# Optimization experiments

Measured on AMD Instinct MI355X. Metric: run time of the kernel, lower is better.

## Reference

```python
import jax, jax.numpy as jnp
import numpy as np

NUM_EXPERTS = 8
HIDDEN = 2048
INTER = 4096
TOKENS = 8192
TOP_K = 2


def setup_inputs() -> dict:
    key = jax.random.key(0)
    ks = jax.random.split(key, 5)
    s = 0.02
    return {
        "x": jax.random.normal(ks[0], (TOKENS, HIDDEN), dtype=jnp.float32),
        "gate_w": jax.random.normal(ks[1], (NUM_EXPERTS, HIDDEN), dtype=jnp.float32) * s,
        "w1": jax.random.normal(ks[2], (NUM_EXPERTS, INTER, HIDDEN), dtype=jnp.float32) * s,
        "w2": jax.random.normal(ks[3], (NUM_EXPERTS, HIDDEN, INTER), dtype=jnp.float32) * s,
        "w3": jax.random.normal(ks[4], (NUM_EXPERTS, INTER, HIDDEN), dtype=jnp.float32) * s,
    }


def reference(x, gate_w, w1, w2, w3):
    # Router: softmax over experts in fp32, then top-2 (no renormalization,
    # matching the torch module which uses the raw top-k softmax probs).
    router_logits = jnp.einsum("th,eh->te", x, gate_w)  # [T, E]
    probs = jax.nn.softmax(router_logits.astype(jnp.float32), axis=1)
    topk_w, topk_idx = jax.lax.top_k(probs, TOP_K)  # [T, K]
    topk_w = topk_w.astype(x.dtype)

    num_experts = w1.shape[0]
    out = jnp.zeros_like(x)
    for e in range(num_experts):
        # Combined routing coefficient for expert e per token (0 if unrouted).
        coef = jnp.sum(jnp.where(topk_idx == e, topk_w, 0.0), axis=1)  # [T]
        # SwiGLU expert FFN: down(silu(gate(x)) * up(x))
        g = jnp.einsum("th,ih->ti", x, w1[e])
        u = jnp.einsum("th,ih->ti", x, w3[e])
        h = jax.nn.silu(g) * u
        y = jnp.einsum("ti,hi->th", h, w2[e])
        out = out + coef[:, None] * y
    return out
```

## Files before the change

### kernel.cpp

```cpp
#include <hip/hip_runtime.h>
#include <stdint.h>
#include <stddef.h>


constexpr int kTokens  = 8192;
constexpr int kHidden  = 2048;
constexpr int kInter   = 4096;
constexpr int kExperts = 8;

constexpr int BM = 128, BN = 128, BK = 64;
constexpr int MAX_MT = (2 * kTokens) / BM + kExperts;

constexpr int BM2 = 256, BN2 = 128, BK2 = 64;
constexpr int MAX_MT2 = (2 * kTokens) / BM2 + kExperts;
constexpr int NT2 = kHidden / BK2;

typedef short bf16x8 __attribute__((ext_vector_type(8)));
typedef float f32x4  __attribute__((ext_vector_type(4)));
typedef unsigned int u32;

__device__ __forceinline__ unsigned short f2bf(float f) {
  union { float f; unsigned u; } v; v.f = f;
  unsigned r = v.u + 0x7FFFu + ((v.u >> 16) & 1u);
  return (unsigned short)(r >> 16);
}

__device__ __forceinline__ void gload16(const void* g, void* l) {
  __builtin_amdgcn_global_load_lds(
      (const __attribute__((address_space(1))) u32*)g,
      (__attribute__((address_space(3))) u32*)l, 16, 0, 0);
}

__global__ __launch_bounds__(256) void convert_w(
    const float* __restrict__ src, unsigned short* __restrict__ dst,
    int lp, int lq, int K, long nchunks)
{
  long stride = (long)gridDim.x * blockDim.x;
  for (long g = blockIdx.x * (long)blockDim.x + threadIdx.x; g < nchunks; g += stride) {
    int  l   = (int)(g & 1023);
    long blk = g >> 10;
    int  q   = (int)(blk & ((1 << lq) - 1));
    long ep  = blk >> lq;
    int  p   = (int)(ep & ((1 << lp) - 1));
    int  e   = (int)(ep >> lp);
    int r = l >> 3, cs = l & 7, c = cs ^ (r & 7);
    size_t soff = (((size_t)(e << lp) + p) * 128 + r) * (size_t)K + (size_t)q * 64 + c * 8;
    float4 v0 = *reinterpret_cast<const float4*>(src + soff);
    float4 v1 = *reinterpret_cast<const float4*>(src + soff + 4);
    uint4 o;
    o.x = (u32)f2bf(v0.x) | ((u32)f2bf(v0.y) << 16);
    o.y = (u32)f2bf(v0.z) | ((u32)f2bf(v0.w) << 16);
    o.z = (u32)f2bf(v1.x) | ((u32)f2bf(v1.y) << 16);
    o.w = (u32)f2bf(v1.z) | ((u32)f2bf(v1.w) << 16);
    *reinterpret_cast<uint4*>(dst + g * 8) = o;
  }
}

__global__ __launch_bounds__(256) void moe_router(
    const float* __restrict__ x, const float* __restrict__ gate_w,
    unsigned short* __restrict__ xb, int* __restrict__ counts,
    int* __restrict__ list_idx, float* __restrict__ list_w)
{
  const int lane = threadIdx.x & 63;
  const int wave = threadIdx.x >> 6;
  const int t = blockIdx.x * 4 + wave;

  float acc[kExperts];
#pragma unroll
  for (int e = 0; e < kExperts; ++e) acc[e] = 0.f;

  const float4* xrow = reinterpret_cast<const float4*>(x + (size_t)t * kHidden);
#pragma unroll
  for (int j = 0; j < 8; ++j) {
    float4 xv = xrow[j * 64 + lane];
    uint2 pk;
    pk.x = (u32)f2bf(xv.x) | ((u32)f2bf(xv.y) << 16);
    pk.y = (u32)f2bf(xv.z) | ((u32)f2bf(xv.w) << 16);
    *reinterpret_cast<uint2*>(xb + (size_t)t * kHidden + j * 256 + lane * 4) = pk;
#pragma unroll
    for (int e = 0; e < kExperts; ++e) {
      float4 gv = reinterpret_cast<const float4*>(gate_w + (size_t)e * kHidden)[j * 64 + lane];
      acc[e] += xv.x * gv.x + xv.y * gv.y + xv.z * gv.z + xv.w * gv.w;
    }
  }
#pragma unroll
  for (int e = 0; e < kExperts; ++e) {
#pragma unroll
    for (int m = 32; m >= 1; m >>= 1) acc[e] += __shfl_xor(acc[e], m);
  }
  if (lane == 0) {
    float mx = acc[0];
#pragma unroll
    for (int e = 1; e < kExperts; ++e) mx = fmaxf(mx, acc[e]);
    float p[kExperts]; float s = 0.f;
#pragma unroll
    for (int e = 0; e < kExperts; ++e) { p[e] = __expf(acc[e] - mx); s += p[e]; }
    float inv = 1.f / s;
    int i1 = 0; float v1 = p[0];
#pragma unroll
    for (int e = 1; e < kExperts; ++e) if (p[e] > v1) { v1 = p[e]; i1 = e; }
    int i2 = (i1 == 0) ? 1 : 0; float v2 = p[i2];
#pragma unroll
    for (int e = 0; e < kExperts; ++e) {
      if (e == i1 || e == i2) continue;
      if (p[e] > v2) { v2 = p[e]; i2 = e; }
    }
    int s1 = atomicAdd(&counts[i1], 1);
    list_idx[i1 * kTokens + s1] = t;
    list_w [i1 * kTokens + s1] = v1 * inv;
    int s2 = atomicAdd(&counts[i2], 1);
    list_idx[i2 * kTokens + s2] = t;
    list_w [i2 * kTokens + s2] = v2 * inv;
  }
}

__device__ __forceinline__ bool map_tile(const int* __restrict__ counts, int mt,
                                         int& e, int& lm, int& sb, int& ne)
{
  int tb = 0; sb = 0;
  for (e = 0; e < kExperts; ++e) {
    ne = counts[e];
    int tiles = (ne + BM - 1) / BM;
    if (mt < tb + tiles) { lm = mt - tb; return true; }
    tb += tiles; sb += ne;
  }
  return false;
}

__device__ __forceinline__ bool map_tile2(const int* __restrict__ counts, int mt,
                                          int& e, int& lm, int& sb, int& ne)
{
  int tb = 0; sb = 0;
  for (e = 0; e < kExperts; ++e) {
    ne = counts[e];
    int tiles = (ne + BM2 - 1) / BM2;
    if (mt < tb + tiles) { lm = mt - tb; return true; }
    tb += tiles; sb += ne;
  }
  return false;
}

__global__ __launch_bounds__(512, 2) void moe_gu2(
    const unsigned short* __restrict__ xb,
    const unsigned short* __restrict__ w1b, const unsigned short* __restrict__ w3b,
    const int* __restrict__ counts, const int* __restrict__ list_idx,
    unsigned short* __restrict__ hbuf)
{
  __shared__ unsigned short lds[65536];
  __shared__ int toks[BM2];

  const int tid = threadIdx.x;
  const int nt  = blockIdx.x / MAX_MT2;
  const int mt  = blockIdx.x % MAX_MT2;

  int e, lm, sb, ne;
  if (!map_tile2(counts, mt, e, lm, sb, ne)) return;
  const int row0 = lm * BM2;

  if (tid < BM2) {
    int lr = row0 + tid;
    toks[tid] = list_idx[e * kTokens + ((lr < ne) ? lr : 0)];
  }
  __syncthreads();

  const int lane = tid & 63;
  const int w    = tid >> 6;
  const int wr   = w >> 2;
  const int wc   = w & 3;

  const unsigned short* srcA[2][2];
  const unsigned short* srcB1[2];
  const unsigned short* srcB3[2];
  {
    const size_t bb = ((size_t)(e * (kInter / BN2) + nt) * (kHidden / BK2)) * 1024;
#pragma unroll
    for (int i = 0; i < 2; ++i) {
      int l = (w * 2 + i) * 64 + lane;
      int r = l >> 3, cs = l & 7, c = cs ^ (r & 7);
#pragma unroll
      for (int h = 0; h < 2; ++h)
        srcA[h][i] = xb + (size_t)toks[h * 128 + r] * kHidden + c * 8;
      srcB1[i] = w1b + (bb + l) * 8;
      srcB3[i] = w3b + (bb + l) * 8;
    }
  }

  f32x4 accG[8][2], accU[8][2];
  const f32x4 zero = {0.f, 0.f, 0.f, 0.f};
#pragma unroll
  for (int m = 0; m < 8; ++m)
#pragma unroll
    for (int n = 0; n < 2; ++n) { accG[m][n] = zero; accU[m][n] = zero; }

#pragma unroll
  for (int i = 0; i < 2; ++i) gload16(srcA[0][i], &lds[0 * 8192 + (w * 2 + i) * 512]);
#pragma unroll
  for (int i = 0; i < 2; ++i) gload16(srcA[1][i], &lds[1 * 8192 + (w * 2 + i) * 512]);
#pragma unroll
  for (int i = 0; i < 2; ++i) gload16(srcB1[i], &lds[32768 + (w * 2 + i) * 512]);
#pragma unroll
  for (int i = 0; i < 2; ++i) gload16(srcB3[i], &lds[49152 + (w * 2 + i) * 512]);
  asm volatile("s_waitcnt vmcnt(2)" ::: "memory");
  __builtin_amdgcn_sched_barrier(0);
  __builtin_amdgcn_s_barrier();

  for (int t = 0; t < NT2; ++t) {
    const int cb = t & 1, nb = cb ^ 1;
    const int tn = (t + 1 < NT2) ? (t + 1) : (NT2 - 1);
    const int Acur = (cb * 2 + wr) * 8192;
    const int B1c  = 32768 + cb * 8192;
    const int B3c  = 49152 + cb * 8192;
    const int An0  = (nb * 2 + 0) * 8192;
    const int An1  = (nb * 2 + 1) * 8192;
    const int B1n  = 32768 + nb * 8192;
    const int B3n  = 49152 + nb * 8192;

    bf16x8 a0[4][2], a1[4][2];
    {
      bf16x8 b1f[2][2];
#pragma unroll
      for (int m = 0; m < 4; ++m) {
        const int r = m * 16 + (lane & 15);
#pragma unroll
        for (int kk = 0; kk < 2; ++kk) {
          const int cq = kk * 4 + (lane >> 4);
          a0[m][kk] = *reinterpret_cast<const bf16x8*>(&lds[Acur + r * 64 + ((cq ^ (r & 7)) << 3)]);
        }
      }
#pragma unroll
      for (int n = 0; n < 2; ++n) {
        const int r = wc * 32 + n * 16 + (lane & 15);
#pragma unroll
        for (int kk = 0; kk < 2; ++kk) {
          const int cq = kk * 4 + (lane >> 4);
          b1f[n][kk] = *reinterpret_cast<const bf16x8*>(&lds[B1c + r * 64 + ((cq ^ (r & 7)) << 3)]);
        }
      }
#pragma unroll
      for (int i = 0; i < 2; ++i) gload16(srcA[0][i] + tn * 64, &lds[An0 + (w * 2 + i) * 512]);
      __builtin_amdgcn_s_setprio(1);
#pragma unroll
      for (int m = 0; m < 4; ++m)
#pragma unroll
        for (int n = 0; n < 2; ++n)
#pragma unroll
          for (int kk = 0; kk < 2; ++kk)
            accG[m][n] = __builtin_amdgcn_mfma_f32_16x16x32_bf16(a0[m][kk], b1f[n][kk], accG[m][n], 0, 0, 0);
      __builtin_amdgcn_s_setprio(0);
      __builtin_amdgcn_sched_barrier(0);
      __builtin_amdgcn_s_barrier();

#pragma unroll
      for (int m = 0; m < 4; ++m) {
        const int r = 64 + m * 16 + (lane & 15);
#pragma unroll
        for (int kk = 0; kk < 2; ++kk) {
          const int cq = kk * 4 + (lane >> 4);
          a1[m][kk] = *reinterpret_cast<const bf16x8*>(&lds[Acur + r * 64 + ((cq ^ (r & 7)) << 3)]);
        }
      }
#pragma unroll
      for (int i = 0; i < 2; ++i) gload16(srcA[1][i] + tn * 64, &lds[An1 + (w * 2 + i) * 512]);
      __builtin_amdgcn_s_setprio(1);
#pragma unroll
      for (int m = 0; m < 4; ++m)
#pragma unroll
        for (int n = 0; n < 2; ++n)
#pragma unroll
          for (int kk = 0; kk < 2; ++kk)
            accG[4 + m][n] = __builtin_amdgcn_mfma_f32_16x16x32_bf16(a1[m][kk], b1f[n][kk], accG[4 + m][n], 0, 0, 0);
      __builtin_amdgcn_s_setprio(0);
      __builtin_amdgcn_sched_barrier(0);
      asm volatile("s_waitcnt vmcnt(4)" ::: "memory");
      __builtin_amdgcn_s_barrier();
    }
    {
      bf16x8 b3f[2][2];
#pragma unroll
      for (int n = 0; n < 2; ++n) {
        const int r = wc * 32 + n * 16 + (lane & 15);
#pragma unroll
        for (int kk = 0; kk < 2; ++kk) {
          const int cq = kk * 4 + (lane >> 4);
          b3f[n][kk] = *reinterpret_cast<const bf16x8*>(&lds[B3c + r * 64 + ((cq ^ (r & 7)) << 3)]);
        }
      }
#pragma unroll
      for (int i = 0; i < 2; ++i) gload16(srcB1[i] + (size_t)tn * 8192, &lds[B1n + (w * 2 + i) * 512]);
      __builtin_amdgcn_s_setprio(1);
#pragma unroll
      for (int m = 0; m < 4; ++m)
#pragma unroll
        for (int n = 0; n < 2; ++n)
#pragma unroll
          for (int kk = 0; kk < 2; ++kk)
            accU[m][n] = __builtin_amdgcn_mfma_f32_16x16x32_bf16(a0[m][kk], b3f[n][kk], accU[m][n], 0, 0, 0);
      __builtin_amdgcn_s_setprio(0);
      __builtin_amdgcn_sched_barrier(0);
      __builtin_amdgcn_s_barrier();

#pragma unroll
      for (int i = 0; i < 2; ++i) gload16(srcB3[i] + (size_t)tn * 8192, &lds[B3n + (w * 2 + i) * 512]);
      __builtin_amdgcn_s_setprio(1);
#pragma unroll
      for (int m = 0; m < 4; ++m)
#pragma unroll
        for (int n = 0; n < 2; ++n)
#pragma unroll
          for (int kk = 0; kk < 2; ++kk)
            accU[4 + m][n] = __builtin_amdgcn_mfma_f32_16x16x32_bf16(a1[m][kk], b3f[n][kk], accU[4 + m][n], 0, 0, 0);
      __builtin_amdgcn_s_setprio(0);
      __builtin_amdgcn_sched_barrier(0);
      asm volatile("s_waitcnt vmcnt(2)" ::: "memory");
      __builtin_amdgcn_s_barrier();
    }
  }

#pragma unroll
  for (int am = 0; am < 8; ++am) {
#pragma unroll
    for (int r = 0; r < 4; ++r) {
      int rloc = wr * 128 + am * 16 + ((lane >> 4) * 4) + r;
      int lrow = row0 + rloc;
      if (lrow < ne) {
        size_t base = (size_t)(sb + lrow) * kInter + (size_t)nt * BN2 + wc * 32 + (lane & 15);
#pragma unroll
        for (int n = 0; n < 2; ++n) {
          float g = accG[am][n][r];
          float u = accU[am][n][r];
          float hv = (g / (1.f + __expf(-g))) * u;
          hbuf[base + n * 16] = f2bf(hv);
        }
      }
    }
  }
}

__global__ __launch_bounds__(256, 3) void moe_y(
    const unsigned short* __restrict__ hbuf,
    const unsigned short* __restrict__ w2b,
    const int* __restrict__ counts, const int* __restrict__ list_idx,
    const float* __restrict__ list_w,
    float* __restrict__ out)
{
  __shared__ unsigned short As[BM * BK];
  __shared__ unsigned short Bs[BN * BK];
  __shared__ int   toks[BM];
  __shared__ float cofs[BM];

  const int tid = threadIdx.x;
  const int nt  = blockIdx.x / MAX_MT;
  const int mt  = blockIdx.x % MAX_MT;

  int e, lm, sb, ne;
  if (!map_tile(counts, mt, e, lm, sb, ne)) return;
  const int row0 = lm * BM;

  if (tid < BM) {
    int lr = row0 + tid;
    bool v = lr < ne;
    toks[tid] = v ? list_idx[e * kTokens + lr] : 0;
    cofs[tid] = v ? list_w [e * kTokens + lr] : 0.f;
  }
  __syncthreads();

  const int lane = tid & 63;
  const int w = tid >> 6;
  const int wr = w >> 1, wc = w & 1;

  const unsigned short* srcA[4];
  const unsigned short* srcB2[4];
  const size_t bbase = ((size_t)(e * (kHidden / BN) + nt) * (kInter / BK)) * 1024;
#pragma unroll
  for (int i = 0; i < 4; ++i) {
    int l = (w * 4 + i) * 64 + lane;
    int r = l >> 3, cs = l & 7, c = cs ^ (r & 7);
    srcA[i]  = hbuf + (size_t)(sb + row0 + r) * kInter + c * 8;
    srcB2[i] = w2b  + (bbase + l) * 8;
  }

  f32x4 acc[4][4];
  const f32x4 zero = {0.f, 0.f, 0.f, 0.f};
#pragma unroll
  for (int m = 0; m < 4; ++m)
#pragma unroll
    for (int n = 0; n < 4; ++n) acc[m][n] = zero;

  for (int ks = 0; ks < kInter / BK; ++ks) {
#pragma unroll
    for (int i = 0; i < 4; ++i) {
      gload16(srcA[i]  + ks * BK,           &As[(w * 4 + i) * 512]);
      gload16(srcB2[i] + (size_t)ks * 8192, &Bs[(w * 4 + i) * 512]);
    }
    __syncthreads();
#pragma unroll
    for (int kk = 0; kk < 2; ++kk) {
      const int cq = kk * 4 + (lane >> 4);
      bf16x8 a[4], b[4];
#pragma unroll
      for (int m = 0; m < 4; ++m) {
        int row = wr * 64 + m * 16 + (lane & 15);
        a[m] = *reinterpret_cast<const bf16x8*>(&As[row * 64 + ((cq ^ (row & 7)) << 3)]);
      }
#pragma unroll
      for (int n = 0; n < 4; ++n) {
        int row = wc * 64 + n * 16 + (lane & 15);
        b[n] = *reinterpret_cast<const bf16x8*>(&Bs[row * 64 + ((cq ^ (row & 7)) << 3)]);
      }
#pragma unroll
      for (int m = 0; m < 4; ++m)
#pragma unroll
        for (int n = 0; n < 4; ++n)
          acc[m][n] = __builtin_amdgcn_mfma_f32_16x16x32_bf16(a[m], b[n], acc[m][n], 0, 0, 0);
    }
    __syncthreads();
  }

#pragma unroll
  for (int m = 0; m < 4; ++m) {
#pragma unroll
    for (int r = 0; r < 4; ++r) {
      int rloc = wr * 64 + m * 16 + ((lane >> 4) * 4) + r;
      if (row0 + rloc < ne) {
        float cf = cofs[rloc];
        size_t obase = (size_t)toks[rloc] * kHidden + (size_t)nt * BN + wc * 64 + (lane & 15);
#pragma unroll
        for (int n = 0; n < 4; ++n)
          atomicAdd(&out[obase + n * 16], cf * acc[m][n][r]);
      }
    }
  }
}

__global__ __launch_bounds__(256, 2) void moe_gu_f32(
    const unsigned short* __restrict__ xb,
    const float* __restrict__ w1, const float* __restrict__ w3,
    const int* __restrict__ counts, const int* __restrict__ list_idx,
    unsigned short* __restrict__ hbuf)
{
  __shared__ unsigned short As [BM * BK];
  __shared__ unsigned short B1s[BN * BK];
  __shared__ unsigned short B3s[BN * BK];
  __shared__ int toks[BM];

  const int tid = threadIdx.x;
  const int nt  = blockIdx.x / MAX_MT;
  const int mt  = blockIdx.x % MAX_MT;

  int e, lm, sb, ne;
  if (!map_tile(counts, mt, e, lm, sb, ne)) return;
  const int row0 = lm * BM;

  if (tid < BM) {
    int lr = row0 + tid;
    toks[tid] = list_idx[e * kTokens + ((lr < ne) ? lr : 0)];
  }
  __syncthreads();

  const unsigned short* aptr[4];
#pragma unroll
  for (int i = 0; i < 4; ++i) {
    int chunk = i * 256 + tid;
    int r = chunk >> 3, c8 = chunk & 7;
    aptr[i] = xb + (size_t)toks[r] * kHidden + c8 * 8;
  }
  const float* w1e = w1 + (size_t)e * kInter * kHidden;
  const float* w3e = w3 + (size_t)e * kInter * kHidden;

  f32x4 accG[4][4], accU[4][4];
  const f32x4 zero = {0.f, 0.f, 0.f, 0.f};
#pragma unroll
  for (int m = 0; m < 4; ++m)
#pragma unroll
    for (int n = 0; n < 4; ++n) { accG[m][n] = zero; accU[m][n] = zero; }

  const int lane = tid & 63;
  const int wr = (tid >> 6) >> 1;
  const int wc = (tid >> 6) & 1;

  for (int k0 = 0; k0 < kHidden; k0 += BK) {
#pragma unroll
    for (int i = 0; i < 4; ++i) {
      int chunk = i * 256 + tid;
      uint4 v = *reinterpret_cast<const uint4*>(aptr[i] + k0);
      *reinterpret_cast<uint4*>(&As[chunk * 8]) = v;
    }
#pragma unroll
    for (int i = 0; i < 8; ++i) {
      int c = i * 256 + tid;
      int rowB = c >> 4, c16 = c & 15;
      size_t off = ((size_t)(nt * BN + rowB)) * kHidden + k0 + c16 * 4;
      float4 v1 = *reinterpret_cast<const float4*>(w1e + off);
      float4 v3 = *reinterpret_cast<const float4*>(w3e + off);
      uint2 p1, p3;
      p1.x = (u32)f2bf(v1.x) | ((u32)f2bf(v1.y) << 16);
      p1.y = (u32)f2bf(v1.z) | ((u32)f2bf(v1.w) << 16);
      p3.x = (u32)f2bf(v3.x) | ((u32)f2bf(v3.y) << 16);
      p3.y = (u32)f2bf(v3.z) | ((u32)f2bf(v3.w) << 16);
      *reinterpret_cast<uint2*>(&B1s[rowB * BK + c16 * 4]) = p1;
      *reinterpret_cast<uint2*>(&B3s[rowB * BK + c16 * 4]) = p3;
    }
    __syncthreads();
#pragma unroll
    for (int kk = 0; kk < 2; ++kk) {
      const int klo = kk * 32 + (lane >> 4) * 8;
      bf16x8 a[4], b1v[4], b3v[4];
#pragma unroll
      for (int m = 0; m < 4; ++m)
        a[m] = *reinterpret_cast<const bf16x8*>(&As[(wr * 64 + m * 16 + (lane & 15)) * BK + klo]);
#pragma unroll
      for (int n = 0; n < 4; ++n) {
// ... 72 lines not shown
  const int wc = (tid >> 6) & 1;

  for (int k0 = 0; k0 < kInter; k0 += BK) {
#pragma unroll
    for (int i = 0; i < 4; ++i) {
      int chunk = i * 256 + tid;
      int r = chunk >> 3, c8 = chunk & 7;
      uint4 v = *reinterpret_cast<const uint4*>(arow + (size_t)r * kInter + k0 + c8 * 8);
      *reinterpret_cast<uint4*>(&As[chunk * 8]) = v;
    }
#pragma unroll
    for (int i = 0; i < 8; ++i) {
      int c = i * 256 + tid;
      int rowB = c >> 4, c16 = c & 15;
      size_t off = ((size_t)(nt * BN + rowB)) * kInter + k0 + c16 * 4;
      float4 v2 = *reinterpret_cast<const float4*>(w2e + off);
      uint2 p2;
      p2.x = (u32)f2bf(v2.x) | ((u32)f2bf(v2.y) << 16);
      p2.y = (u32)f2bf(v2.z) | ((u32)f2bf(v2.w) << 16);
      *reinterpret_cast<uint2*>(&Bs[rowB * BK + c16 * 4]) = p2;
    }
    __syncthreads();
#pragma unroll
    for (int kk = 0; kk < 2; ++kk) {
      const int klo = kk * 32 + (lane >> 4) * 8;
      bf16x8 a[4], b[4];
#pragma unroll
      for (int m = 0; m < 4; ++m)
        a[m] = *reinterpret_cast<const bf16x8*>(&As[(wr * 64 + m * 16 + (lane & 15)) * BK + klo]);
#pragma unroll
      for (int n = 0; n < 4; ++n)
        b[n] = *reinterpret_cast<const bf16x8*>(&Bs[(wc * 64 + n * 16 + (lane & 15)) * BK + klo]);
#pragma unroll
      for (int m = 0; m < 4; ++m)
#pragma unroll
        for (int n = 0; n < 4; ++n)
          acc[m][n] = __builtin_amdgcn_mfma_f32_16x16x32_bf16(a[m], b[n], acc[m][n], 0, 0, 0);
    }
    __syncthreads();
  }
#pragma unroll
  for (int m = 0; m < 4; ++m) {
#pragma unroll
    for (int r = 0; r < 4; ++r) {
      int rloc = wr * 64 + m * 16 + ((lane >> 4) * 4) + r;
      if (row0 + rloc < ne) {
        float cf = cofs[rloc];
        size_t obase = (size_t)toks[rloc] * kHidden + (size_t)nt * BN + wc * 64 + (lane & 15);
#pragma unroll
        for (int n = 0; n < 4; ++n)
          atomicAdd(&out[obase + n * 16], cf * acc[m][n][r]);
      }
    }
  }
}

extern "C" void kernel_launch(void* const* d_in, const int* in_sizes, int n_in,
                              void* d_out, int out_size, void* d_ws, size_t ws_size,
                              hipStream_t stream)
{
  const float* x      = (const float*)d_in[0];
  const float* gate_w = (const float*)d_in[1];
  const float* w1     = (const float*)d_in[2];
  const float* w2     = (const float*)d_in[3];
  const float* w3     = (const float*)d_in[4];
  float* out = (float*)d_out;

  char* ws = (char*)d_ws;
  const size_t MiB = 1ull << 20;
  int*   counts   = (int*)(ws);
  int*   list_idx = (int*)(ws + 1024);
  float* list_w   = (float*)(ws + 1024 + kExperts * kTokens * 4);

  hipMemsetAsync(counts, 0, 1024, stream);
  hipMemsetAsync(out, 0, (size_t)kTokens * kHidden * sizeof(float), stream);

  if (ws_size >= 418 * MiB) {
    unsigned short* xb   = (unsigned short*)(ws + 1 * MiB);
    unsigned short* w1b  = (unsigned short*)(ws + 33 * MiB);
    unsigned short* w3b  = (unsigned short*)(ws + 161 * MiB);
    unsigned short* hbuf = (unsigned short*)(ws + 289 * MiB);
    unsigned short* w2b  = w1b;

    const long nch = (long)kExperts * (kInter / BN) * (kHidden / BK) * 1024;
    convert_w<<<4096, 256, 0, stream>>>(w1, w1b, 5, 5, kHidden, nch);
    convert_w<<<4096, 256, 0, stream>>>(w3, w3b, 5, 5, kHidden, nch);
    moe_router<<<kTokens / 4, 256, 0, stream>>>(x, gate_w, xb, counts, list_idx, list_w);
    moe_gu2<<<(kInter / BN2) * MAX_MT2, 512, 0, stream>>>(xb, w1b, w3b, counts, list_idx, hbuf);
    convert_w<<<4096, 256, 0, stream>>>(w2, w2b, 4, 6, kInter, nch);
    moe_y<<<(kHidden / BN) * MAX_MT, 256, 0, stream>>>(hbuf, w2b, counts, list_idx, list_w, out);
  } else {
    unsigned short* xb   = (unsigned short*)(ws + 1 * MiB);
    unsigned short* hbuf = (unsigned short*)(ws + 36 * MiB);
    moe_router<<<kTokens / 4, 256, 0, stream>>>(x, gate_w, xb, counts, list_idx, list_w);
    moe_gu_f32<<<(kInter / BN) * MAX_MT, 256, 0, stream>>>(xb, w1, w3, counts, list_idx, hbuf);
    moe_y_f32 <<<(kHidden / BN) * MAX_MT, 256, 0, stream>>>(hbuf, w2, counts, list_idx, list_w, out);
  }
}
```

Measured before the change: 1.492 ms.

## Pipeline down-projection with 256-row tiles, triple-buffered LDS, and reordered grid

Replaces the down-projection kernel with a 512-thread, 256x128 tile version. It uses triple-buffered LDS, async global-to-LDS prefetch two steps ahead, and one barrier per k-step instead of two syncthreads. The gate/up kernel is unrolled by two with fewer barriers and a reordered prefetch schedule. Both grids now put the N panel as the fast index, so blocks sharing the same token rows run together and reuse them from cache. This gives more overlap and reuse, but raises register and LDS pressure, and the fixed vmcnt counts must match the reordered loads.

Result: slower. 1.797 ms (median of 2 runs) (+20.5%).

```diff
diff --git a/kernel.cpp b/kernel.cpp
--- a/kernel.cpp
+++ b/kernel.cpp
@@ -11,9 +11,13 @@
 constexpr int BM = 128, BN = 128, BK = 64;
 constexpr int MAX_MT = (2 * kTokens) / BM + kExperts;
 
-constexpr int BM2 = 256, BN2 = 128, BK2 = 64;
+constexpr int BM2 = 256, BN2 = 128;
 constexpr int MAX_MT2 = (2 * kTokens) / BM2 + kExperts;
-constexpr int NT2 = kHidden / BK2;
+constexpr int NT2 = kHidden / BK;
+constexpr int NTY = kInter / BK;
+constexpr int NPAN_GU = kInter / BN2;
+constexpr int NPAN_Y  = kHidden / BN2;
+constexpr int kSlotCap = 16512;
 
 typedef short bf16x8 __attribute__((ext_vector_type(8)));
 typedef float f32x4  __attribute__((ext_vector_type(4)));
@@ -150,8 +154,8 @@
   __shared__ int toks[BM2];
 
   const int tid = threadIdx.x;
-  const int nt  = blockIdx.x / MAX_MT2;
-  const int mt  = blockIdx.x % MAX_MT2;
+  const int nt  = blockIdx.x % NPAN_GU;
+  const int mt  = blockIdx.x / NPAN_GU;
 
   int e, lm, sb, ne;
   if (!map_tile2(counts, mt, e, lm, sb, ne)) return;
@@ -172,7 +176,7 @@
   const unsigned short* srcB1[2];
   const unsigned short* srcB3[2];
   {
-    const size_t bb = ((size_t)(e * (kInter / BN2) + nt) * (kHidden / BK2)) * 1024;
+    const size_t bb = ((size_t)(e * NPAN_GU + nt) * NT2) * 1024;
 #pragma unroll
     for (int i = 0; i < 2; ++i) {
       int l = (w * 2 + i) * 64 + lane;
@@ -204,20 +208,22 @@
   __builtin_amdgcn_sched_barrier(0);
   __builtin_amdgcn_s_barrier();
 
-  for (int t = 0; t < NT2; ++t) {
-    const int cb = t & 1, nb = cb ^ 1;
-    const int tn = (t + 1 < NT2) ? (t + 1) : (NT2 - 1);
-    const int Acur = (cb * 2 + wr) * 8192;
-    const int B1c  = 32768 + cb * 8192;
-    const int B3c  = 49152 + cb * 8192;
-    const int An0  = (nb * 2 + 0) * 8192;
-    const int An1  = (nb * 2 + 1) * 8192;
-    const int B1n  = 32768 + nb * 8192;
-    const int B3n  = 49152 + nb * 8192;
-
-    bf16x8 a0[4][2], a1[4][2];
-    {
-      bf16x8 b1f[2][2];
+  for (int t2 = 0; t2 < NT2; t2 += 2) {
+#pragma unroll
+    for (int u = 0; u < 2; ++u) {
+      const int t  = t2 + u;
+      const int cb = u, nb = u ^ 1;
+      const int tn = (t + 1 < NT2) ? (t + 1) : (NT2 - 1);
+      const int Acur = (cb * 2 + wr) * 8192;
+      const int B1c  = 32768 + cb * 8192;
+      const int B3c  = 49152 + cb * 8192;
+      const int An0  = (nb * 2 + 0) * 8192;
+      const int An1  = (nb * 2 + 1) * 8192;
+      const int B1n  = 32768 + nb * 8192;
+      const int B3n  = 49152 + nb * 8192;
+
+      bf16x8 a0[4][2], a1[4][2], b1f[2][2], b3f[2][2];
+
 #pragma unroll
       for (int m = 0; m < 4; ++m) {
         const int r = m * 16 + (lane & 15);
@@ -237,7 +243,10 @@
         }
       }
 #pragma unroll
-      for (int i = 0; i < 2; ++i) gload16(srcA[0][i] + tn * 64, &lds[An0 + (w * 2 + i) * 512]);
+      for (int i = 0; i < 2; ++i) {
+        gload16(srcA[0][i] + tn * BK, &lds[An0 + (w * 2 + i) * 512]);
+        gload16(srcA[1][i] + tn * BK, &lds[An1 + (w * 2 + i) * 512]);
+      }
       __builtin_amdgcn_s_setprio(1);
 #pragma unroll
       for (int m = 0; m < 4; ++m)
@@ -248,7 +257,6 @@
             accG[m][n] = __builtin_amdgcn_mfma_f32_16x16x32_bf16(a0[m][kk], b1f[n][kk], accG[m][n], 0, 0, 0);
       __builtin_amdgcn_s_setprio(0);
       __builtin_amdgcn_sched_barrier(0);
-      __builtin_amdgcn_s_barrier();
 
 #pragma unroll
       for (int m = 0; m < 4; ++m) {
@@ -260,7 +268,8 @@
         }
       }
 #pragma unroll
-      for (int i = 0; i < 2; ++i) gload16(srcA[1][i] + tn * 64, &lds[An1 + (w * 2 + i) * 512]);
+      for (int i = 0; i < 2; ++i)
+        gload16(srcB1[i] + (size_t)tn * 8192, &lds[B1n + (w * 2 + i) * 512]);
       __builtin_amdgcn_s_setprio(1);
 #pragma unroll
       for (int m = 0; m < 4; ++m)
@@ -271,11 +280,9 @@
             accG[4 + m][n] = __builtin_amdgcn_mfma_f32_16x16x32_bf16(a1[m][kk], b1f[n][kk], accG[4 + m][n], 0, 0, 0);
       __builtin_amdgcn_s_setprio(0);
       __builtin_amdgcn_sched_barrier(0);
-      asm volatile("s_waitcnt vmcnt(4)" ::: "memory");
+      asm volatile("s_waitcnt vmcnt(6)" ::: "memory");
       __builtin_amdgcn_s_barrier();
-    }
-    {
-      bf16x8 b3f[2][2];
+
 #pragma unroll
       for (int n = 0; n < 2; ++n) {
         const int r = wc * 32 + n * 16 + (lane & 15);
@@ -286,7 +293,8 @@
         }
       }
 #pragma unroll
-      for (int i = 0; i < 2; ++i) gload16(srcB1[i] + (size_t)tn * 8192, &lds[B1n + (w * 2 + i) * 512]);
+      for (int i = 0; i < 2; ++i)
+        gload16(srcB3[i] + (size_t)tn * 8192, &lds[B3n + (w * 2 + i) * 512]);
       __builtin_amdgcn_s_setprio(1);
 #pragma unroll
       for (int m = 0; m < 4; ++m)
@@ -297,10 +305,6 @@
             accU[m][n] = __builtin_amdgcn_mfma_f32_16x16x32_bf16(a0[m][kk], b3f[n][kk], accU[m][n], 0, 0, 0);
       __builtin_amdgcn_s_setprio(0);
       __builtin_amdgcn_sched_barrier(0);
-      __builtin_amdgcn_s_barrier();
-
-#pragma unroll
-      for (int i = 0; i < 2; ++i) gload16(srcB3[i] + (size_t)tn * 8192, &lds[B3n + (w * 2 + i) * 512]);
       __builtin_amdgcn_s_setprio(1);
 #pragma unroll
       for (int m = 0; m < 4; ++m)
@@ -336,27 +340,94 @@
   }
 }
 
-__global__ __launch_bounds__(256, 3) void moe_y(
+#define Y_TILE(T, CB)                                                          \
+  {                                                                            \
+    const int tn  = ((T) + 2 < NTY) ? ((T) + 2) : (NTY - 1);                   \
+    const int cob = (CB) * 24576;                                              \
+    const int nxb = (((CB) + 2) % 3) * 24576;                                  \
+    bf16x8 a0[4][2], a1[4][2], bfv[2][2];                                      \
+    _Pragma("unroll")                                                          \
+    for (int m = 0; m < 4; ++m) {                                              \
+      const int r = m * 16 + (lane & 15);                                      \
+      _Pragma("unroll")                                                        \
+      for (int kk = 0; kk < 2; ++kk) {                                         \
+        const int cq = kk * 4 + (lane >> 4);                                   \
+        a0[m][kk] = *reinterpret_cast<const bf16x8*>(                          \
+            &lds[cob + wr * 8192 + r * 64 + ((cq ^ (r & 7)) << 3)]);           \
+      }                                                                        \
+    }                                                                          \
+    _Pragma("unroll")                                                          \
+    for (int n = 0; n < 2; ++n) {                                              \
+      const int r = wc * 32 + n * 16 + (lane & 15);                            \
+      _Pragma("unroll")                                                        \
+      for (int kk = 0; kk < 2; ++kk) {                                         \
+        const int cq = kk * 4 + (lane >> 4);                                   \
+        bfv[n][kk] = *reinterpret_cast<const bf16x8*>(                         \
+            &lds[cob + 16384 + r * 64 + ((cq ^ (r & 7)) << 3)]);               \
+      }                                                                        \
+    }                                                                          \
+    _Pragma("unroll")                                                          \
+    for (int i = 0; i < 2; ++i) {                                              \
+      gload16(srcA[0][i] + (size_t)tn * BK, &lds[nxb + (w * 2 + i) * 512]);    \
+      gload16(srcB[i] + (size_t)tn * 8192, &lds[nxb + 16384 + (w * 2 + i) * 512]); \
+    }                                                                          \
+    __builtin_amdgcn_s_setprio(1);                                             \
+    _Pragma("unroll")                                                          \
+    for (int m = 0; m < 4; ++m)                                                \
+      _Pragma("unroll")                                                        \
+      for (int n = 0; n < 2; ++n)                                              \
+        _Pragma("unroll")                                                      \
+        for (int kk = 0; kk < 2; ++kk)                                         \
+          acc[m][n] = __builtin_amdgcn_mfma_f32_16x16x32_bf16(a0[m][kk], bfv[n][kk], acc[m][n], 0, 0, 0); \
+    __builtin_amdgcn_s_setprio(0);                                             \
+    __builtin_amdgcn_sched_barrier(0);                                         \
+    _Pragma("unroll")                                                          \
+    for (int m = 0; m < 4; ++m) {                                              \
+      const int r = 64 + m * 16 + (lane & 15);                                 \
+      _Pragma("unroll")                                                        \
+      for (int kk = 0; kk < 2; ++kk) {                                         \
+        const int cq = kk * 4 + (lane >> 4);                                   \
+        a1[m][kk] = *reinterpret_cast<const bf16x8*>(                          \
+            &lds[cob + wr * 8192 + r * 64 + ((cq ^ (r & 7)) << 3)]);           \
+      }                                                                        \
+    }                                                                          \
+    _Pragma("unroll")                                                          \
+    for (int i = 0; i < 2; ++i)                                                \
+      gload16(srcA[1][i] + (size_t)tn * BK, &lds[nxb + 8192 + (w * 2 + i) * 512]); \
+    __builtin_amdgcn_s_setprio(1);                                             \
+    _Pragma("unroll")                                                          \
+    for (int m = 0; m < 4; ++m)                                                \
+      _Pragma("unroll")                                                        \
+      for (int n = 0; n < 2; ++n)                                              \
+        _Pragma("unroll")                                                      \
+        for (int kk = 0; kk < 2; ++kk)                                         \
+          acc[4 + m][n] = __builtin_amdgcn_mfma_f32_16x16x32_bf16(a1[m][kk], bfv[n][kk], acc[4 + m][n], 0, 0, 0); \
+    __builtin_amdgcn_s_setprio(0);                                             \
+    __builtin_amdgcn_sched_barrier(0);                                         \
+    asm volatile("s_waitcnt vmcnt(6)" ::: "memory");                           \
+    __builtin_amdgcn_s_barrier();                                              \
+  }
+
+__global__ __launch_bounds__(512, 2) void moe_y2(
     const unsigned short* __restrict__ hbuf,
     const unsigned short* __restrict__ w2b,
     const int* __restrict__ counts, const int* __restrict__ list_idx,
     const float* __restrict__ list_w,
     float* __restrict__ out)
 {
-  __shared__ unsigned short As[BM * BK];
-  __shared__ unsigned short Bs[BN * BK];
-  __shared__ int   toks[BM];
-  __shared__ float cofs[BM];
+  __shared__ unsigned short lds[73728];
+  __shared__ int   toks[BM2];
+  __shared__ float cofs[BM2];
 
   const int tid = threadIdx.x;
-  const int nt  = blockIdx.x / MAX_MT;
-  const int mt  = blockIdx.x % MAX_MT;
+  const int nt  = blockIdx.x % NPAN_Y;
+  const int mt  = blockIdx.x / NPAN_Y;
 
   int e, lm, sb, ne;
-  if (!map_tile(counts, mt, e, lm, sb, ne)) return;
-  const int row0 = lm * BM;
-
-  if (tid < BM) {
+  if (!map_tile2(counts, mt, e, lm, sb, ne)) return;
+  const int row0 = lm * BM2;
+
+  if (tid < BM2) {
     int lr = row0 + tid;
     bool v = lr < ne;
     toks[tid] = v ? list_idx[e * kTokens + lr] : 0;
@@ -365,68 +436,69 @@
   __syncthreads();
 
   const int lane = tid & 63;
-  const int w = tid >> 6;
-  const int wr = w >> 1, wc = w & 1;
-
-  const unsigned short* srcA[4];
-  const unsigned short* srcB2[4];
-  const size_t bbase = ((size_t)(e * (kHidden / BN) + nt) * (kInter / BK)) * 1024;
-#pragma unroll
-  for (int i = 0; i < 4; ++i) {
-    int l = (w * 4 + i) * 64 + lane;
-    int r = l >> 3, cs = l & 7, c = cs ^ (r & 7);
-    srcA[i]  = hbuf + (size_t)(sb + row0 + r) * kInter + c * 8;
-    srcB2[i] = w2b  + (bbase + l) * 8;
-  }
-
-  f32x4 acc[4][4];
+  const int w    = tid >> 6;
+  const int wr   = w >> 2;
+  const int wc   = w & 3;
+
+  const unsigned short* srcA[2][2];
+  const unsigned short* srcB[2];
+  {
+    const size_t bb = ((size_t)(e * NPAN_Y + nt) * NTY) * 1024;
+#pragma unroll
+    for (int i = 0; i < 2; ++i) {
+      int l = (w * 2 + i) * 64 + lane;
+      int r = l >> 3, cs = l & 7, c = cs ^ (r & 7);
+#pragma unroll
+      for (int h = 0; h < 2; ++h) {
+        int rg = sb + row0 + h * 128 + r;
+        if (rg > kSlotCap - 1) rg = kSlotCap - 1;
+        srcA[h][i] = hbuf + (size_t)rg * kInter + c * 8;
+      }
+      srcB[i] = w2b + (bb + l) * 8;
+    }
+  }
+
+  f32x4 acc[8][2];
   const f32x4 zero = {0.f, 0.f, 0.f, 0.f};
 #pragma unroll
-  for (int m = 0; m < 4; ++m)
-#pragma unroll
-    for (int n = 0; n < 4; ++n) acc[m][n] = zero;
-
-  for (int ks = 0; ks < kInter / BK; ++ks) {
-#pragma unroll
-    for (int i = 0; i < 4; ++i) {
-      gload16(srcA[i]  + ks * BK,           &As[(w * 4 + i) * 512]);
-      gload16(srcB2[i] + (size_t)ks * 8192, &Bs[(w * 4 + i) * 512]);
-    }
-    __syncthreads();
-#pragma unroll
-    for (int kk = 0; kk < 2; ++kk) {
-      const int cq = kk * 4 + (lane >> 4);
-      bf16x8 a[4], b[4];
-#pragma unroll
-      for (int m = 0; m < 4; ++m) {
-        int row = wr * 64 + m * 16 + (lane & 15);
-        a[m] = *reinterpret_cast<const bf16x8*>(&As[row * 64 + ((cq ^ (row & 7)) << 3)]);
-      }
-#pragma unroll
-      for (int n = 0; n < 4; ++n) {
-        int row = wc * 64 + n * 16 + (lane & 15);
-        b[n] = *reinterpret_cast<const bf16x8*>(&Bs[row * 64 + ((cq ^ (row & 7)) << 3)]);
-      }
-#pragma unroll
-      for (int m = 0; m < 4; ++m)
-#pragma unroll
-        for (int n = 0; n < 4; ++n)
-          acc[m][n] = __builtin_amdgcn_mfma_f32_16x16x32_bf16(a[m], b[n], acc[m][n], 0, 0, 0);
-    }
-    __syncthreads();
-  }
-
-#pragma unroll
-  for (int m = 0; m < 4; ++m) {
+  for (int m = 0; m < 8; ++m)
+#pragma unroll
+    for (int n = 0; n < 2; ++n) acc[m][n] = zero;
+
+#pragma unroll
+  for (int t = 0; t < 2; ++t) {
+    const int bo = t * 24576;
+#pragma unroll
+    for (int i = 0; i < 2; ++i) {
+      gload16(srcA[0][i] + (size_t)t * BK, &lds[bo + (w * 2 + i) * 512]);
+      gload16(srcB[i] + (size_t)t * 8192, &lds[bo + 16384 + (w * 2 + i) * 512]);
+    }
+#pragma unroll
+    for (int i = 0; i < 2; ++i)
+      gload16(srcA[1][i] + (size_t)t * BK, &lds[bo + 8192 + (w * 2 + i) * 512]);
+  }
+  asm volatile("s_waitcnt vmcnt(6)" ::: "memory");
+  __builtin_amdgcn_sched_barrier(0);
+  __builtin_amdgcn_s_barrier();
+
+  Y_TILE(0, 0)
+  for (int t3 = 1; t3 < NTY; t3 += 3) {
+    Y_TILE(t3, 1)
+    Y_TILE(t3 + 1, 2)
+    Y_TILE(t3 + 2, 0)
+  }
+
+#pragma unroll
+  for (int am = 0; am < 8; ++am) {
 #pragma unroll
     for (int r = 0; r < 4; ++r) {
-      int rloc = wr * 64 + m * 16 + ((lane >> 4) * 4) + r;
+      int rloc = wr * 128 + am * 16 + ((lane >> 4) * 4) + r;
       if (row0 + rloc < ne) {
         float cf = cofs[rloc];
-        size_t obase = (size_t)toks[rloc] * kHidden + (size_t)nt * BN + wc * 64 + (lane & 15);
-#pragma unroll
-        for (int n = 0; n < 4; ++n)
-          atomicAdd(&out[obase + n * 16], cf * acc[m][n][r]);
+        size_t obase = (size_t)toks[rloc] * kHidden + (size_t)nt * BN2 + wc * 32 + (lane & 15);
+#pragma unroll
+        for (int n = 0; n < 2; ++n)
+          atomicAdd(&out[obase + n * 16], cf * acc[am][n][r]);
       }
     }
   }
@@ -669,9 +741,9 @@
     convert_w<<<4096, 256, 0, stream>>>(w1, w1b, 5, 5, kHidden, nch);
     convert_w<<<4096, 256, 0, stream>>>(w3, w3b, 5, 5, kHidden, nch);
     moe_router<<<kTokens / 4, 256, 0, stream>>>(x, gate_w, xb, counts, list_idx, list_w);
-    moe_gu2<<<(kInter / BN2) * MAX_MT2, 512, 0, stream>>>(xb, w1b, w3b, counts, list_idx, hbuf);
+    moe_gu2<<<MAX_MT2 * NPAN_GU, 512, 0, stream>>>(xb, w1b, w3b, counts, list_idx, hbuf);
     convert_w<<<4096, 256, 0, stream>>>(w2, w2b, 4, 6, kInter, nch);
-    moe_y<<<(kHidden / BN) * MAX_MT, 256, 0, stream>>>(hbuf, w2b, counts, list_idx, list_w, out);
+    moe_y2<<<MAX_MT2 * NPAN_Y, 512, 0, stream>>>(hbuf, w2b, counts, list_idx, list_w, out);
   } else {
     unsigned short* xb   = (unsigned short*)(ws + 1 * MiB);
     unsigned short* hbuf = (unsigned short*)(ws + 36 * MiB);
```

## Pre-layout weights in MFMA fragment order and stream B operands straight to registers

Applied to the files above, without the earlier changes.

Weight conversion now writes bf16 weights in MFMA fragment order, so each lane can load its B fragments directly from global memory into registers. This removes the LDS staging for weights in both GEMMs. The gate/up kernel issues gate and up MFMAs interleaved in a single double-buffered loop, with only the activations double-buffered in LDS. The down-projection kernel moves to 256-row tiles with 512 threads and uses the same register-prefetch scheme. The cost is higher register pressure and uncoalesced-per-wave-but-contiguous global weight reads that rely on cache reuse across blocks.

Measured after the change: 1.587 ms. +6.4%, slower.

```diff
diff --git a/kernel.cpp b/kernel.cpp
--- a/kernel.cpp
+++ b/kernel.cpp
@@ -11,9 +11,13 @@
 constexpr int BM = 128, BN = 128, BK = 64;
 constexpr int MAX_MT = (2 * kTokens) / BM + kExperts;
 
-constexpr int BM2 = 256, BN2 = 128, BK2 = 64;
+constexpr int BM2 = 256, BN2 = 128;
 constexpr int MAX_MT2 = (2 * kTokens) / BM2 + kExperts;
-constexpr int NT2 = kHidden / BK2;
+constexpr int NT2 = kHidden / BK;
+constexpr int NTY = kInter / BK;
+constexpr int NPAN_GU = kInter / BN2;
+constexpr int NPAN_Y  = kHidden / BN2;
+constexpr int kSlotCap = 16512;
 
 typedef short bf16x8 __attribute__((ext_vector_type(8)));
 typedef float f32x4  __attribute__((ext_vector_type(4)));
@@ -31,20 +35,23 @@
       (__attribute__((address_space(3))) u32*)l, 16, 0, 0);
 }
 
-__global__ __launch_bounds__(256) void convert_w(
+__global__ __launch_bounds__(256) void convert_w_frag(
     const float* __restrict__ src, unsigned short* __restrict__ dst,
     int lp, int lq, int K, long nchunks)
 {
   long stride = (long)gridDim.x * blockDim.x;
   for (long g = blockIdx.x * (long)blockDim.x + threadIdx.x; g < nchunks; g += stride) {
-    int  l   = (int)(g & 1023);
+    int  c13 = (int)(g & 1023);
     long blk = g >> 10;
     int  q   = (int)(blk & ((1 << lq) - 1));
     long ep  = blk >> lq;
     int  p   = (int)(ep & ((1 << lp) - 1));
     int  e   = (int)(ep >> lp);
-    int r = l >> 3, cs = l & 7, c = cs ^ (r & 7);
-    size_t soff = (((size_t)(e << lp) + p) * 128 + r) * (size_t)K + (size_t)q * 64 + c * 8;
+    int fg = c13 >> 6, l = c13 & 63;
+    int g8 = fg >> 1, kk = fg & 1;
+    int row = g8 * 16 + (l & 15);
+    int kq  = kk * 4 + (l >> 4);
+    size_t soff = (((size_t)(e << lp) + p) * 128 + row) * (size_t)K + (size_t)q * 64 + kq * 8;
     float4 v0 = *reinterpret_cast<const float4*>(src + soff);
     float4 v1 = *reinterpret_cast<const float4*>(src + soff + 4);
     uint4 o;
@@ -140,13 +147,13 @@
   return false;
 }
 
-__global__ __launch_bounds__(512, 2) void moe_gu2(
+__global__ __launch_bounds__(512, 2) void moe_gu3(
     const unsigned short* __restrict__ xb,
     const unsigned short* __restrict__ w1b, const unsigned short* __restrict__ w3b,
     const int* __restrict__ counts, const int* __restrict__ list_idx,
     unsigned short* __restrict__ hbuf)
 {
-  __shared__ unsigned short lds[65536];
+  __shared__ unsigned short As[2][16384];
   __shared__ int toks[BM2];
 
   const int tid = threadIdx.x;
@@ -168,22 +175,21 @@
   const int wr   = w >> 2;
   const int wc   = w & 3;
 
-  const unsigned short* srcA[2][2];
-  const unsigned short* srcB1[2];
-  const unsigned short* srcB3[2];
-  {
-    const size_t bb = ((size_t)(e * (kInter / BN2) + nt) * (kHidden / BK2)) * 1024;
-#pragma unroll
-    for (int i = 0; i < 2; ++i) {
-      int l = (w * 2 + i) * 64 + lane;
-      int r = l >> 3, cs = l & 7, c = cs ^ (r & 7);
-#pragma unroll
-      for (int h = 0; h < 2; ++h)
-        srcA[h][i] = xb + (size_t)toks[h * 128 + r] * kHidden + c * 8;
-      srcB1[i] = w1b + (bb + l) * 8;
-      srcB3[i] = w3b + (bb + l) * 8;
-    }
-  }
+  const unsigned short* srcA[4];
+#pragma unroll
+  for (int i = 0; i < 4; ++i) {
+    int l = (w * 4 + i) * 64 + lane;
+    int r = l >> 3, c = (l & 7) ^ (r & 7);
+    srcA[i] = xb + (size_t)toks[r] * kHidden + c * 8;
+  }
+
+  const size_t tb0 = ((size_t)(e * NPAN_GU + nt)) * NT2 * 8192;
+  int foff[2][2];
+#pragma unroll
+  for (int n = 0; n < 2; ++n)
+#pragma unroll
+    for (int kk = 0; kk < 2; ++kk)
+      foff[n][kk] = (((wc * 2 + n) * 2 + kk) * 64 + lane) * 8;
 
   f32x4 accG[8][2], accU[8][2];
   const f32x4 zero = {0.f, 0.f, 0.f, 0.f};
@@ -192,128 +198,71 @@
 #pragma unroll
     for (int n = 0; n < 2; ++n) { accG[m][n] = zero; accU[m][n] = zero; }
 
-#pragma unroll
-  for (int i = 0; i < 2; ++i) gload16(srcA[0][i], &lds[0 * 8192 + (w * 2 + i) * 512]);
-#pragma unroll
-  for (int i = 0; i < 2; ++i) gload16(srcA[1][i], &lds[1 * 8192 + (w * 2 + i) * 512]);
-#pragma unroll
-  for (int i = 0; i < 2; ++i) gload16(srcB1[i], &lds[32768 + (w * 2 + i) * 512]);
-#pragma unroll
-  for (int i = 0; i < 2; ++i) gload16(srcB3[i], &lds[49152 + (w * 2 + i) * 512]);
-  asm volatile("s_waitcnt vmcnt(2)" ::: "memory");
+  bf16x8 b1a[2][2], b3a[2][2], b1b[2][2], b3b[2][2];
+
+#pragma unroll
+  for (int i = 0; i < 4; ++i) gload16(srcA[i], &As[0][(w * 4 + i) * 512]);
+  __builtin_amdgcn_sched_barrier(0);
+#pragma unroll
+  for (int n = 0; n < 2; ++n)
+#pragma unroll
+    for (int kk = 0; kk < 2; ++kk) {
+      b1a[n][kk] = *reinterpret_cast<const bf16x8*>(w1b + tb0 + foff[n][kk]);
+      b3a[n][kk] = *reinterpret_cast<const bf16x8*>(w3b + tb0 + foff[n][kk]);
+    }
+  asm volatile("s_waitcnt vmcnt(8)" ::: "memory");
   __builtin_amdgcn_sched_barrier(0);
   __builtin_amdgcn_s_barrier();
 
-  for (int t = 0; t < NT2; ++t) {
-    const int cb = t & 1, nb = cb ^ 1;
+  auto tile = [&](int t, int buf,
+                  bf16x8 (&b1c)[2][2], bf16x8 (&b3c)[2][2],
+                  bf16x8 (&b1n)[2][2], bf16x8 (&b3n)[2][2]) {
     const int tn = (t + 1 < NT2) ? (t + 1) : (NT2 - 1);
-    const int Acur = (cb * 2 + wr) * 8192;
-    const int B1c  = 32768 + cb * 8192;
-    const int B3c  = 49152 + cb * 8192;
-    const int An0  = (nb * 2 + 0) * 8192;
-    const int An1  = (nb * 2 + 1) * 8192;
-    const int B1n  = 32768 + nb * 8192;
-    const int B3n  = 49152 + nb * 8192;
-
-    bf16x8 a0[4][2], a1[4][2];
-    {
-      bf16x8 b1f[2][2];
+#pragma unroll
+    for (int i = 0; i < 4; ++i)
+      gload16(srcA[i] + tn * BK, &As[buf ^ 1][(w * 4 + i) * 512]);
+    __builtin_amdgcn_sched_barrier(0);
+    const size_t tbn = tb0 + (size_t)tn * 8192;
+#pragma unroll
+    for (int n = 0; n < 2; ++n)
+#pragma unroll
+      for (int kk = 0; kk < 2; ++kk) {
+        b1n[n][kk] = *reinterpret_cast<const bf16x8*>(w1b + tbn + foff[n][kk]);
+        b3n[n][kk] = *reinterpret_cast<const bf16x8*>(w3b + tbn + foff[n][kk]);
+      }
+#pragma unroll
+    for (int mh = 0; mh < 2; ++mh) {
+      bf16x8 a[4][2];
 #pragma unroll
       for (int m = 0; m < 4; ++m) {
-        const int r = m * 16 + (lane & 15);
+        const int r = wr * 128 + mh * 64 + m * 16 + (lane & 15);
 #pragma unroll
         for (int kk = 0; kk < 2; ++kk) {
           const int cq = kk * 4 + (lane >> 4);
-          a0[m][kk] = *reinterpret_cast<const bf16x8*>(&lds[Acur + r * 64 + ((cq ^ (r & 7)) << 3)]);
+          a[m][kk] = *reinterpret_cast<const bf16x8*>(
+              &As[buf][r * 64 + ((cq ^ (r & 7)) << 3)]);
         }
       }
 #pragma unroll
-      for (int n = 0; n < 2; ++n) {
-        const int r = wc * 32 + n * 16 + (lane & 15);
-#pragma unroll
-        for (int kk = 0; kk < 2; ++kk) {
-          const int cq = kk * 4 + (lane >> 4);
-          b1f[n][kk] = *reinterpret_cast<const bf16x8*>(&lds[B1c + r * 64 + ((cq ^ (r & 7)) << 3)]);
-        }
-      }
-#pragma unroll
-      for (int i = 0; i < 2; ++i) gload16(srcA[0][i] + tn * 64, &lds[An0 + (w * 2 + i) * 512]);
-      __builtin_amdgcn_s_setprio(1);
-#pragma unroll
       for (int m = 0; m < 4; ++m)
 #pragma unroll
         for (int n = 0; n < 2; ++n)
 #pragma unroll
-          for (int kk = 0; kk < 2; ++kk)
-            accG[m][n] = __builtin_amdgcn_mfma_f32_16x16x32_bf16(a0[m][kk], b1f[n][kk], accG[m][n], 0, 0, 0);
-      __builtin_amdgcn_s_setprio(0);
-      __builtin_amdgcn_sched_barrier(0);
-      __builtin_amdgcn_s_barrier();
-
-#pragma unroll
-      for (int m = 0; m < 4; ++m) {
-        const int r = 64 + m * 16 + (lane & 15);
-#pragma unroll
-        for (int kk = 0; kk < 2; ++kk) {
-          const int cq = kk * 4 + (lane >> 4);
-          a1[m][kk] = *reinterpret_cast<const bf16x8*>(&lds[Acur + r * 64 + ((cq ^ (r & 7)) << 3)]);
-        }
-      }
-#pragma unroll
-      for (int i = 0; i < 2; ++i) gload16(srcA[1][i] + tn * 64, &lds[An1 + (w * 2 + i) * 512]);
-      __builtin_amdgcn_s_setprio(1);
-#pragma unroll
-      for (int m = 0; m < 4; ++m)
-#pragma unroll
-        for (int n = 0; n < 2; ++n)
-#pragma unroll
-          for (int kk = 0; kk < 2; ++kk)
-            accG[4 + m][n] = __builtin_amdgcn_mfma_f32_16x16x32_bf16(a1[m][kk], b1f[n][kk], accG[4 + m][n], 0, 0, 0);
-      __builtin_amdgcn_s_setprio(0);
-      __builtin_amdgcn_sched_barrier(0);
-      asm volatile("s_waitcnt vmcnt(4)" ::: "memory");
-      __builtin_amdgcn_s_barrier();
-    }
-    {
-      bf16x8 b3f[2][2];
-#pragma unroll
-      for (int n = 0; n < 2; ++n) {
-        const int r = wc * 32 + n * 16 + (lane & 15);
-#pragma unroll
-        for (int kk = 0; kk < 2; ++kk) {
-          const int cq = kk * 4 + (lane >> 4);
-          b3f[n][kk] = *reinterpret_cast<const bf16x8*>(&lds[B3c + r * 64 + ((cq ^ (r & 7)) << 3)]);
-        }
-      }
-#pragma unroll
-      for (int i = 0; i < 2; ++i) gload16(srcB1[i] + (size_t)tn * 8192, &lds[B1n + (w * 2 + i) * 512]);
-      __builtin_amdgcn_s_setprio(1);
-#pragma unroll
-      for (int m = 0; m < 4; ++m)
-#pragma unroll
-        for (int n = 0; n < 2; ++n)
-#pragma unroll
-          for (int kk = 0; kk < 2; ++kk)
-            accU[m][n] = __builtin_amdgcn_mfma_f32_16x16x32_bf16(a0[m][kk], b3f[n][kk], accU[m][n], 0, 0, 0);
-      __builtin_amdgcn_s_setprio(0);
-      __builtin_amdgcn_sched_barrier(0);
-      __builtin_amdgcn_s_barrier();
-
-#pragma unroll
-      for (int i = 0; i < 2; ++i) gload16(srcB3[i] + (size_t)tn * 8192, &lds[B3n + (w * 2 + i) * 512]);
-      __builtin_amdgcn_s_setprio(1);
-#pragma unroll
-      for (int m = 0; m < 4; ++m)
-#pragma unroll
-        for (int n = 0; n < 2; ++n)
-#pragma unroll
-          for (int kk = 0; kk < 2; ++kk)
-            accU[4 + m][n] = __builtin_amdgcn_mfma_f32_16x16x32_bf16(a1[m][kk], b3f[n][kk], accU[4 + m][n], 0, 0, 0);
-      __builtin_amdgcn_s_setprio(0);
-      __builtin_amdgcn_sched_barrier(0);
-      asm volatile("s_waitcnt vmcnt(2)" ::: "memory");
-      __builtin_amdgcn_s_barrier();
-    }
+          for (int kk = 0; kk < 2; ++kk) {
+            accG[mh * 4 + m][n] = __builtin_amdgcn_mfma_f32_16x16x32_bf16(
+                a[m][kk], b1c[n][kk], accG[mh * 4 + m][n], 0, 0, 0);
+            accU[mh * 4 + m][n] = __builtin_amdgcn_mfma_f32_16x16x32_bf16(
+                a[m][kk], b3c[n][kk], accU[mh * 4 + m][n], 0, 0, 0);
+          }
+    }
+    asm volatile("s_waitcnt vmcnt(8)" ::: "memory");
+    __builtin_amdgcn_sched_barrier(0);
+    __builtin_amdgcn_s_barrier();
+  };
+
+  for (int t2 = 0; t2 < NT2; t2 += 2) {
+    tile(t2,     0, b1a, b3a, b1b, b3b);
+    tile(t2 + 1, 1, b1b, b3b, b1a, b3a);
   }
 
 #pragma unroll
@@ -336,27 +285,26 @@
   }
 }
 
-__global__ __launch_bounds__(256, 3) void moe_y(
+__global__ __launch_bounds__(512, 2) void moe_y3(
     const unsigned short* __restrict__ hbuf,
     const unsigned short* __restrict__ w2b,
     const int* __restrict__ counts, const int* __restrict__ list_idx,
     const float* __restrict__ list_w,
     float* __restrict__ out)
 {
-  __shared__ unsigned short As[BM * BK];
-  __shared__ unsigned short Bs[BN * BK];
-  __shared__ int   toks[BM];
-  __shared__ float cofs[BM];
+  __shared__ unsigned short As[2][16384];
+  __shared__ int   toks[BM2];
+  __shared__ float cofs[BM2];
 
   const int tid = threadIdx.x;
-  const int nt  = blockIdx.x / MAX_MT;
-  const int mt  = blockIdx.x % MAX_MT;
+  const int nt  = blockIdx.x / MAX_MT2;
+  const int mt  = blockIdx.x % MAX_MT2;
 
   int e, lm, sb, ne;
-  if (!map_tile(counts, mt, e, lm, sb, ne)) return;
-  const int row0 = lm * BM;
-
-  if (tid < BM) {
+  if (!map_tile2(counts, mt, e, lm, sb, ne)) return;
+  const int row0 = lm * BM2;
+
+  if (tid < BM2) {
     int lr = row0 + tid;
     bool v = lr < ne;
     toks[tid] = v ? list_idx[e * kTokens + lr] : 0;
@@ -365,19 +313,27 @@
   __syncthreads();
 
   const int lane = tid & 63;
-  const int w = tid >> 6;
-  const int wr = w >> 1, wc = w & 1;
+  const int w    = tid >> 6;
+  const int wr   = w >> 1;
+  const int wc   = w & 1;
 
   const unsigned short* srcA[4];
-  const unsigned short* srcB2[4];
-  const size_t bbase = ((size_t)(e * (kHidden / BN) + nt) * (kInter / BK)) * 1024;
 #pragma unroll
   for (int i = 0; i < 4; ++i) {
     int l = (w * 4 + i) * 64 + lane;
-    int r = l >> 3, cs = l & 7, c = cs ^ (r & 7);
-    srcA[i]  = hbuf + (size_t)(sb + row0 + r) * kInter + c * 8;
-    srcB2[i] = w2b  + (bbase + l) * 8;
-  }
+    int r = l >> 3, c = (l & 7) ^ (r & 7);
+    int rg = sb + row0 + r;
+    if (rg > kSlotCap - 1) rg = kSlotCap - 1;
+    srcA[i] = hbuf + (size_t)rg * kInter + c * 8;
+  }
+
+  const size_t tb0 = ((size_t)(e * NPAN_Y + nt)) * NTY * 8192;
+  int foff[4][2];
+#pragma unroll
+  for (int n = 0; n < 4; ++n)
+#pragma unroll
+    for (int kk = 0; kk < 2; ++kk)
+      foff[n][kk] = (((wc * 4 + n) * 2 + kk) * 64 + lane) * 8;
 
   f32x4 acc[4][4];
   const f32x4 zero = {0.f, 0.f, 0.f, 0.f};
@@ -386,34 +342,57 @@
 #pragma unroll
     for (int n = 0; n < 4; ++n) acc[m][n] = zero;
 
-  for (int ks = 0; ks < kInter / BK; ++ks) {
-#pragma unroll
-    for (int i = 0; i < 4; ++i) {
-      gload16(srcA[i]  + ks * BK,           &As[(w * 4 + i) * 512]);
-      gload16(srcB2[i] + (size_t)ks * 8192, &Bs[(w * 4 + i) * 512]);
-    }
-    __syncthreads();
+  bf16x8 b2a[4][2], b2b[4][2];
+
+#pragma unroll
+  for (int i = 0; i < 4; ++i) gload16(srcA[i], &As[0][(w * 4 + i) * 512]);
+  __builtin_amdgcn_sched_barrier(0);
+#pragma unroll
+  for (int n = 0; n < 4; ++n)
+#pragma unroll
+    for (int kk = 0; kk < 2; ++kk)
+      b2a[n][kk] = *reinterpret_cast<const bf16x8*>(w2b + tb0 + foff[n][kk]);
+  asm volatile("s_waitcnt vmcnt(8)" ::: "memory");
+  __builtin_amdgcn_sched_barrier(0);
+  __builtin_amdgcn_s_barrier();
+
+  auto tile = [&](int t, int buf, bf16x8 (&b2c)[4][2], bf16x8 (&b2n)[4][2]) {
+    const int tn = (t + 1 < NTY) ? (t + 1) : (NTY - 1);
+#pragma unroll
+    for (int i = 0; i < 4; ++i)
+      gload16(srcA[i] + tn * BK, &As[buf ^ 1][(w * 4 + i) * 512]);
+    __builtin_amdgcn_sched_barrier(0);
+    const size_t tbn = tb0 + (size_t)tn * 8192;
+#pragma unroll
+    for (int n = 0; n < 4; ++n)
+#pragma unroll
+      for (int kk = 0; kk < 2; ++kk)
+        b2n[n][kk] = *reinterpret_cast<const bf16x8*>(w2b + tbn + foff[n][kk]);
 #pragma unroll
     for (int kk = 0; kk < 2; ++kk) {
-      const int cq = kk * 4 + (lane >> 4);
-      bf16x8 a[4], b[4];
+      bf16x8 a[4];
 #pragma unroll
       for (int m = 0; m < 4; ++m) {
-        int row = wr * 64 + m * 16 + (lane & 15);
-        a[m] = *reinterpret_cast<const bf16x8*>(&As[row * 64 + ((cq ^ (row & 7)) << 3)]);
-      }
-#pragma unroll
-      for (int n = 0; n < 4; ++n) {
-        int row = wc * 64 + n * 16 + (lane & 15);
-        b[n] = *reinterpret_cast<const bf16x8*>(&Bs[row * 64 + ((cq ^ (row & 7)) << 3)]);
+        const int r = wr * 64 + m * 16 + (lane & 15);
+        const int cq = kk * 4 + (lane >> 4);
+        a[m] = *reinterpret_cast<const bf16x8*>(
+            &As[buf][r * 64 + ((cq ^ (r & 7)) << 3)]);
       }
 #pragma unroll
       for (int m = 0; m < 4; ++m)
 #pragma unroll
         for (int n = 0; n < 4; ++n)
-          acc[m][n] = __builtin_amdgcn_mfma_f32_16x16x32_bf16(a[m], b[n], acc[m][n], 0, 0, 0);
-    }
-    __syncthreads();
+          acc[m][n] = __builtin_amdgcn_mfma_f32_16x16x32_bf16(
+              a[m], b2c[n][kk], acc[m][n], 0, 0, 0);
+    }
+    asm volatile("s_waitcnt vmcnt(8)" ::: "memory");
+    __builtin_amdgcn_sched_barrier(0);
+    __builtin_amdgcn_s_barrier();
+  };
+
+  for (int t2 = 0; t2 < NTY; t2 += 2) {
+    tile(t2,     0, b2a, b2b);
+    tile(t2 + 1, 1, b2b, b2a);
   }
 
 #pragma unroll
@@ -423,7 +402,7 @@
       int rloc = wr * 64 + m * 16 + ((lane >> 4) * 4) + r;
       if (row0 + rloc < ne) {
         float cf = cofs[rloc];
-        size_t obase = (size_t)toks[rloc] * kHidden + (size_t)nt * BN + wc * 64 + (lane & 15);
+        size_t obase = (size_t)toks[rloc] * kHidden + (size_t)nt * BN2 + wc * 64 + (lane & 15);
 #pragma unroll
         for (int n = 0; n < 4; ++n)
           atomicAdd(&out[obase + n * 16], cf * acc[m][n][r]);
@@ -665,13 +644,13 @@
     unsigned short* hbuf = (unsigned short*)(ws + 289 * MiB);
     unsigned short* w2b  = w1b;
 
-    const long nch = (long)kExperts * (kInter / BN) * (kHidden / BK) * 1024;
-    convert_w<<<4096, 256, 0, stream>>>(w1, w1b, 5, 5, kHidden, nch);
-    convert_w<<<4096, 256, 0, stream>>>(w3, w3b, 5, 5, kHidden, nch);
+    const long nch = (long)kExperts * NPAN_GU * NT2 * 1024;
+    convert_w_frag<<<4096, 256, 0, stream>>>(w1, w1b, 5, 5, kHidden, nch);
+    convert_w_frag<<<4096, 256, 0, stream>>>(w3, w3b, 5, 5, kHidden, nch);
     moe_router<<<kTokens / 4, 256, 0, stream>>>(x, gate_w, xb, counts, list_idx, list_w);
-    moe_gu2<<<(kInter / BN2) * MAX_MT2, 512, 0, stream>>>(xb, w1b, w3b, counts, list_idx, hbuf);
-    convert_w<<<4096, 256, 0, stream>>>(w2, w2b, 4, 6, kInter, nch);
-    moe_y<<<(kHidden / BN) * MAX_MT, 256, 0, stream>>>(hbuf, w2b, counts, list_idx, list_w, out);
+    moe_gu3<<<NPAN_GU * MAX_MT2, 512, 0, stream>>>(xb, w1b, w3b, counts, list_idx, hbuf);
+    convert_w_frag<<<4096, 256, 0, stream>>>(w2, w2b, 4, 6, kInter, nch);
+    moe_y3<<<NPAN_Y * MAX_MT2, 512, 0, stream>>>(hbuf, w2b, counts, list_idx, list_w, out);
   } else {
     unsigned short* xb   = (unsigned short*)(ws + 1 * MiB);
     unsigned short* hbuf = (unsigned short*)(ws + 36 * MiB);
```
